# Performance work log

Hardware: AMD Instinct MI355X
Metric: run time of the kernel (lower is better)

Reference implementation:

```python
import jax, jax.numpy as jnp
import numpy as np

C = 1.0          # curvature
EPS = 1e-6
BETA = 0.5       # residual_beta
N_NODES = 65536
N_EDGES = 1048576
D = 128          # pure feature dim; hyperboloid coords are D+1


def _mink_dot(x, y):
    # Lorentz inner product <x,y>_L = -x0*y0 + sum_i xi*yi
    return jnp.sum(x * y, axis=-1) - 2.0 * x[..., 0] * y[..., 0]


def _proj(x, c=C):
    # project onto hyperboloid: x0 = sqrt(1/c + ||x_s||^2)
    xs = x[..., 1:]
    x0 = jnp.sqrt(1.0 / c + jnp.sum(xs * xs, axis=-1, keepdims=True))
    return jnp.concatenate([x0, xs], axis=-1)


def _log0_pure(x, c=C):
    # log map at origin, returning the pure (spatial) tangent part (..., D)
    sc = jnp.sqrt(c)
    x0 = x[..., :1]
    xs = x[..., 1:]
    xn = jnp.sqrt(jnp.maximum(jnp.sum(xs * xs, axis=-1, keepdims=True), EPS * EPS))
    theta = jnp.arccosh(jnp.maximum(sc * x0, 1.0 + EPS))
    return (theta / (sc * xn)) * xs


def _exp0_pure(v, c=C):
    # exp map at origin from pure tangent vector v (..., D) -> (..., D+1)
    sc = jnp.sqrt(c)
    vn = jnp.sqrt(jnp.maximum(jnp.sum(v * v, axis=-1, keepdims=True), EPS * EPS))
    a = sc * vn
    x0 = jnp.cosh(a) / sc
    xs = jnp.sinh(a) * v / a
    return jnp.concatenate([x0, xs], axis=-1)


def _log(x, y, c=C):
    # general Lorentz log map log_x(y)
    sc = jnp.sqrt(c)
    alpha = jnp.maximum(-c * _mink_dot(x, y), 1.0 + EPS)[..., None]
    u = y - alpha * x
    un = jnp.sqrt(jnp.maximum(_mink_dot(u, u)[..., None], EPS * EPS))
    dist = jnp.arccosh(alpha) / sc
    return dist * u / un


def _exp(x, v, c=C):
    # general Lorentz exp map exp_x(v)
    sc = jnp.sqrt(c)
    vn = jnp.sqrt(jnp.maximum(_mink_dot(v, v)[..., None], EPS * EPS))
    a = sc * vn
    return jnp.cosh(a) * x + jnp.sinh(a) * v / a


def _hgcn_layer(x, src, dst, W, b):
    n = x.shape[0]
    # HyperbolicLinear (basepoint=origin): tangent linear map then exp back
    h = _exp0_pure(_log0_pure(x) @ W.T + b)
    # mean aggregation in tangent space at origin (self-loops already in src/dst)
    t = _log0_pure(h)                                   # (N, D)
    s = jax.ops.segment_sum(t[src], dst, num_segments=n)  # (N, D)
    cnt = jax.ops.segment_sum(jnp.ones((src.shape[0],), t.dtype), dst, num_segments=n)
    mean = s / jnp.maximum(cnt, 1.0)[:, None]
    agg = _proj(_exp0_pure(mean))                        # normalize_after_aggregation
    # hyperbolic ReLU (basepoint=origin)
    act = _exp0_pure(jax.nn.relu(_log0_pure(agg)))
    # geodesic residual: exp_residual(beta * log_residual(act))
    act = _exp(x, BETA * _log(x, act))
    return _proj(act)


def setup_inputs() -> dict:
    key = jax.random.key(0)
    k1, k2, k3, k4, k5, k6 = jax.random.split(key, 6)
    xs = 0.1 * jax.random.normal(k1, (N_NODES, D), dtype=jnp.float32)
    x = _proj(jnp.concatenate([jnp.zeros((N_NODES, 1), jnp.float32), xs], axis=-1))
    edge_index = jax.random.randint(k2, (2, N_EDGES), 0, N_NODES, dtype=jnp.int32)
    scale = 1.0 / np.sqrt(D)
    W1 = scale * jax.random.normal(k3, (D, D), dtype=jnp.float32)
    b1 = 0.01 * jax.random.normal(k4, (D,), dtype=jnp.float32)
    W2 = scale * jax.random.normal(k5, (D, D), dtype=jnp.float32)
    b2 = 0.01 * jax.random.normal(k6, (D,), dtype=jnp.float32)
    return {"x": x, "edge_index": edge_index, "W1": W1, "b1": b1, "W2": W2, "b2": b2}


def reference(x, edge_index, W1, b1, W2, b2):
    n = x.shape[0]
    loops = jnp.arange(n, dtype=edge_index.dtype)
    src = jnp.concatenate([edge_index[0], loops])
    dst = jnp.concatenate([edge_index[1], loops])
    h = _hgcn_layer(x, src, dst, W1, b1)
    h = _proj(h)  # normalize_between_layers
    h = _hgcn_layer(h, src, dst, W2, b2)
    return h
```

## Files before the change

kernel.cpp:

```cpp
#include <hip/hip_runtime.h>
#include <hip/hip_bf16.h>
#include <hip/hip_fp16.h>
#include <math.h>

#define NN 65536
#define NE 1048576
#define D 128
#define DP 129
#define EPSF 1e-6f
#define TILE 4096

typedef _Float16 half8 __attribute__((ext_vector_type(8)));
typedef float floatx16 __attribute__((ext_vector_type(16)));
typedef float floatx2 __attribute__((ext_vector_type(2)));

__device__ __forceinline__ float frcp(float x) { return __builtin_amdgcn_rcpf(x); }
__device__ __forceinline__ float fsqrt(float x) { return __builtin_amdgcn_sqrtf(x); }
__device__ __forceinline__ float facosh(float x) {
    return __logf(x + fsqrt(fmaxf(x * x - 1.0f, 0.0f)));
}


__global__ __launch_bounds__(256) void k_bzero(int* __restrict__ bcnt) {
    bcnt[threadIdx.x] = 0;
}

__global__ __launch_bounds__(256) void k_bhist(const int* __restrict__ dst, int E,
                                               int* __restrict__ bcnt) {
    __shared__ int lh[256];
    int t = threadIdx.x;
    lh[t] = 0;
    __syncthreads();
    int base = blockIdx.x * TILE;
    #pragma unroll
    for (int k = 0; k < 16; ++k) {
        int i = base + k * 256 + t;
        if (i < E) atomicAdd(&lh[dst[i] >> 8], 1);
    }
    __syncthreads();
    if (lh[t]) atomicAdd(&bcnt[t], lh[t]);
}

__global__ __launch_bounds__(256) void k_bscan(const int* __restrict__ bcnt,
                                               int* __restrict__ bbase,
                                               int* __restrict__ bcur) {
    __shared__ int sh[256];
    int t = threadIdx.x;
    int v = bcnt[t];
    sh[t] = v;
    __syncthreads();
    for (int o = 1; o < 256; o <<= 1) {
        int u = (t >= o) ? sh[t - o] : 0;
        __syncthreads();
        sh[t] += u;
        __syncthreads();
    }
    int ex = sh[t] - v;
    bbase[t] = ex;
    bcur[t] = ex;
}

__global__ __launch_bounds__(256) void k_bsplit(const int* __restrict__ src,
                                                const int* __restrict__ dst, int E,
                                                int* __restrict__ bcur,
                                                unsigned int* __restrict__ ebuf) {
    __shared__ int lh[256];
    __shared__ int gres[256];
    int t = threadIdx.x;
    lh[t] = 0;
    __syncthreads();
    int base = blockIdx.x * TILE;
    unsigned int pk[16];
    int bk[16], rk[16];
    #pragma unroll
    for (int k = 0; k < 16; ++k) {
        int i = base + k * 256 + t;
        if (i < E) {
            int d = dst[i];
            int b = d >> 8;
            bk[k] = b;
            pk[k] = ((unsigned)(d & 255) << 16) | (unsigned)src[i];
            rk[k] = atomicAdd(&lh[b], 1);
        } else {
            bk[k] = -1; rk[k] = 0; pk[k] = 0;
        }
    }
    __syncthreads();
    gres[t] = lh[t] ? atomicAdd(&bcur[t], lh[t]) : 0;
    __syncthreads();
    #pragma unroll
    for (int k = 0; k < 16; ++k) {
        if (bk[k] >= 0) ebuf[gres[bk[k]] + rk[k]] = pk[k];
    }
}

__global__ __launch_bounds__(256) void k_csr(const unsigned int* __restrict__ ebuf,
                                             const int* __restrict__ bcnt,
                                             const int* __restrict__ bbase,
                                             int* __restrict__ deg,
                                             int* __restrict__ off,
                                             int* __restrict__ ssrc) {
    __shared__ int lh[256];
    __shared__ int sc[256];
    __shared__ int lcur[256];
    int t = threadIdx.x;
    int b = blockIdx.x;
    int start = bbase[b];
    int cnt = bcnt[b];
    lh[t] = 0;
    __syncthreads();
    for (int i = t; i < cnt; i += 256) {
        unsigned int e = ebuf[start + i];
        atomicAdd(&lh[e >> 16], 1);
    }
    __syncthreads();
    int v = lh[t];
    sc[t] = v;
    __syncthreads();
    for (int o = 1; o < 256; o <<= 1) {
        int u = (t >= o) ? sc[t - o] : 0;
        __syncthreads();
        sc[t] += u;
        __syncthreads();
    }
    int ex = sc[t] - v;
    int node = (b << 8) + t;
    deg[node] = v;
    off[node] = start + ex;
    lcur[t] = ex;
    __syncthreads();
    for (int i = t; i < cnt; i += 256) {
        unsigned int e = ebuf[start + i];
        int d = e >> 16;
        int r = atomicAdd(&lcur[d], 1);
        ssrc[start + r] = (int)(e & 0xFFFFu);
    }
}

template <bool FROM_F16>
__global__ __launch_bounds__(256) void k_gemm(const float* __restrict__ x,
                                              const _Float16* __restrict__ y,
                                              const float* __restrict__ W,
                                              const float* __restrict__ bias,
                                              unsigned int* __restrict__ zw) {
    __shared__ _Float16 Ah[128 * 128];
    __shared__ _Float16 Wh[128 * 128];
    int t = threadIdx.x;
    int w = t >> 6;
    int l = t & 63;
    int j = l & 31;
    int hi = l >> 5;
    int r0 = blockIdx.x * 128;

    #pragma unroll
    for (int i = 0; i < 8; ++i) {
        int c = i * 256 + t;
        int row = c >> 4, slot = c & 15;
        const float4* wp = (const float4*)(W + row * 128 + slot * 8);
        float4 w0 = wp[0], w1 = wp[1];
        half8 hv;
        hv[0] = (_Float16)w0.x; hv[1] = (_Float16)w0.y;
        hv[2] = (_Float16)w0.z; hv[3] = (_Float16)w0.w;
        hv[4] = (_Float16)w1.x; hv[5] = (_Float16)w1.y;
        hv[6] = (_Float16)w1.z; hv[7] = (_Float16)w1.w;
        *(half8*)&Wh[row * 128 + ((slot ^ (row & 15)) << 3)] = hv;
    }

    if constexpr (FROM_F16) {
        #pragma unroll
        for (int i = 0; i < 8; ++i) {
            int c = i * 256 + t;
            int row = c >> 4, slot = c & 15;
            half8 hv = *(const half8*)(y + (size_t)(r0 + row) * 128 + slot * 8);
            *(half8*)&Ah[row * 128 + ((slot ^ (row & 15)) << 3)] = hv;
        }
    } else {
        for (int it = 0; it < 16; ++it) {
            int rl = w * 32 + it * 2 + hi;
            const float* xr = x + (size_t)(r0 + rl) * DP;
            float x0 = xr[0];
            float a0 = xr[1 + j];
            float a1 = xr[33 + j];
            float a2 = xr[65 + j];
            float a3 = xr[97 + j];
            float ss = a0 * a0 + a1 * a1 + a2 * a2 + a3 * a3;
            ss += __shfl_xor(ss, 1);
            ss += __shfl_xor(ss, 2);
            ss += __shfl_xor(ss, 4);
            ss += __shfl_xor(ss, 8);
            ss += __shfl_xor(ss, 16);
            float xn = fsqrt(fmaxf(ss, EPSF * EPSF));
            float theta = facosh(fmaxf(x0, 1.0f + EPSF));
            float f = theta * frcp(xn);
            int base = rl * 128;
            int swz = (rl & 15) << 3;
            Ah[base + ((j)      ^ swz)] = (_Float16)(f * a0);
            Ah[base + ((j + 32) ^ swz)] = (_Float16)(f * a1);
            Ah[base + ((j + 64) ^ swz)] = (_Float16)(f * a2);
            Ah[base + ((j + 96) ^ swz)] = (_Float16)(f * a3);
        }
    }
    __syncthreads();

    int rA = w * 32 + j;
    int swzj = (j & 15) << 3;
    const _Float16* Abase = &Ah[rA * 128];
    const _Float16* B0 = &Wh[(j)*128];
    const _Float16* B1 = &Wh[(j + 32) * 128];
    const _Float16* B2 = &Wh[(j + 64) * 128];
    const _Float16* B3 = &Wh[(j + 96) * 128];

    float bv0 = bias[j], bv1 = bias[j + 32], bv2 = bias[j + 64], bv3 = bias[j + 96];
    floatx16 acc0, acc1, acc2, acc3;
    #pragma unroll
    for (int q = 0; q < 16; ++q) {
        acc0[q] = bv0; acc1[q] = bv1; acc2[q] = bv2; acc3[q] = bv3;
    }

    #pragma unroll
    for (int ks = 0; ks < 8; ++ks) {
        int kh = (ks * 16 + hi * 8) ^ swzj;
        half8 a  = *(const half8*)(Abase + kh);
        half8 b0 = *(const half8*)(B0 + kh);
        half8 b1 = *(const half8*)(B1 + kh);
        half8 b2 = *(const half8*)(B2 + kh);
        half8 b3 = *(const half8*)(B3 + kh);
        acc0 = __builtin_amdgcn_mfma_f32_32x32x16_f16(a, b0, acc0, 0, 0, 0);
        acc1 = __builtin_amdgcn_mfma_f32_32x32x16_f16(a, b1, acc1, 0, 0, 0);
        acc2 = __builtin_amdgcn_mfma_f32_32x32x16_f16(a, b2, acc2, 0, 0, 0);
        acc3 = __builtin_amdgcn_mfma_f32_32x32x16_f16(a, b3, acc3, 0, 0, 0);
    }

    #pragma unroll
    for (int q = 0; q < 16; ++q) {
        int row = r0 + w * 32 + (q & 3) + 8 * (q >> 2) + 4 * hi;
        unsigned int u = 0;
        u = (unsigned int)__builtin_amdgcn_cvt_pk_fp8_f32(acc0[q], acc1[q], (int)u, false);
        u = (unsigned int)__builtin_amdgcn_cvt_pk_fp8_f32(acc2[q], acc3[q], (int)u, true);
        zw[(size_t)row * 32 + j] = u;
    }
}

template <bool WRITE_Y>
__global__ __launch_bounds__(256) void k_agg(const unsigned short* __restrict__ zs,
                                             const float* xin,
                                             const int* __restrict__ off,
                                             const int* __restrict__ deg,
                                             const int* __restrict__ ssrc,
                                             float* out,
                                             _Float16* __restrict__ y2) {
    int wave = threadIdx.x >> 6, lane = threadIdx.x & 63;
    int node = __builtin_amdgcn_readfirstlane(blockIdx.x * 4 + wave);
    int c0 = (lane >> 1) + ((lane & 1) << 6);

    floatx2 acc0 = __builtin_amdgcn_cvt_pk_f32_fp8((int)zs[(size_t)node * 64 + lane], false);
    floatx2 acc1 = {0.f, 0.f}, acc2 = {0.f, 0.f}, acc3 = {0.f, 0.f};

    int start = __builtin_amdgcn_readfirstlane(off[node]);
    int dg = __builtin_amdgcn_readfirstlane(deg[node]);

    for (int c = 0; c < dg; c += 64) {
        int rem = dg - c;
        int m = rem < 64 ? rem : 64;
        int sv = ssrc[start + c + lane];
        int j = 0;
        for (; j + 7 < m; j += 8) {
            int s0 = __builtin_amdgcn_readlane(sv, j + 0);
            int s1 = __builtin_amdgcn_readlane(sv, j + 1);
            int s2 = __builtin_amdgcn_readlane(sv, j + 2);
            int s3 = __builtin_amdgcn_readlane(sv, j + 3);
            int s4 = __builtin_amdgcn_readlane(sv, j + 4);
            int s5 = __builtin_amdgcn_readlane(sv, j + 5);
            int s6 = __builtin_amdgcn_readlane(sv, j + 6);
            int s7 = __builtin_amdgcn_readlane(sv, j + 7);
            floatx2 v0 = __builtin_amdgcn_cvt_pk_f32_fp8((int)zs[(size_t)s0 * 64 + lane], false);
            floatx2 v1 = __builtin_amdgcn_cvt_pk_f32_fp8((int)zs[(size_t)s1 * 64 + lane], false);
            floatx2 v2 = __builtin_amdgcn_cvt_pk_f32_fp8((int)zs[(size_t)s2 * 64 + lane], false);
            floatx2 v3 = __builtin_amdgcn_cvt_pk_f32_fp8((int)zs[(size_t)s3 * 64 + lane], false);
            floatx2 v4 = __builtin_amdgcn_cvt_pk_f32_fp8((int)zs[(size_t)s4 * 64 + lane], false);
            floatx2 v5 = __builtin_amdgcn_cvt_pk_f32_fp8((int)zs[(size_t)s5 * 64 + lane], false);
            floatx2 v6 = __builtin_amdgcn_cvt_pk_f32_fp8((int)zs[(size_t)s6 * 64 + lane], false);
            floatx2 v7 = __builtin_amdgcn_cvt_pk_f32_fp8((int)zs[(size_t)s7 * 64 + lane], false);
            acc0 += v0; acc1 += v1; acc2 += v2; acc3 += v3;
            acc0 += v4; acc1 += v5; acc2 += v6; acc3 += v7;
        }
        for (; j < m; ++j) {
            int s = __builtin_amdgcn_readlane(sv, j);
            floatx2 v = __builtin_amdgcn_cvt_pk_f32_fp8((int)zs[(size_t)s * 64 + lane], false);
            acc0 += v;
        }
    }
    floatx2 accT = (acc0 + acc1) + (acc2 + acc3);
    float ax = accT.x, ay = accT.y;

    float inv = frcp((float)(dg + 1));
    float rx = fmaxf(ax * inv, 0.0f);
    float ry = fmaxf(ay * inv, 0.0f);

    float ss = rx * rx + ry * ry;
    #pragma unroll
    for (int o = 1; o < 64; o <<= 1) ss += __shfl_xor(ss, o);
    float av = fsqrt(fmaxf(ss, EPSF * EPSF));
    float t1 = __expf(av);
    float t1i = frcp(t1);
    float shf = 0.5f * (t1 - t1i) * frcp(av);
    float act0 = 0.5f * (t1 + t1i);
    float asx = shf * rx, asy = shf * ry;

    const float* xr = xin + (size_t)node * DP;
    float x0 = xr[0];
    float xsx = xr[1 + c0];
    float xsy = xr[33 + c0];

    float dot = asx * xsx + asy * xsy;
    #pragma unroll
    for (int o = 1; o < 64; o <<= 1) dot += __shfl_xor(dot, o);
    float mink = dot - act0 * x0;
    float alpha = fmaxf(-mink, 1.0f + EPSF);

    float u0 = act0 - alpha * x0;
    float ux = asx - alpha * xsx;
    float uy = asy - alpha * xsy;
    float uss = ux * ux + uy * uy;
    #pragma unroll
    for (int o = 1; o < 64; o <<= 1) uss += __shfl_xor(uss, o);
    float uu = uss - u0 * u0;
    float un = fsqrt(fmaxf(uu, EPSF * EPSF));

    float d = facosh(alpha);
    float a2 = 0.5f * d;
    float t2 = __expf(a2);
    float t2i = frcp(t2);
    float ch2 = 0.5f * (t2 + t2i);
    float sh2 = 0.5f * (t2 - t2i) * frcp(un);

    float ox = ch2 * xsx + sh2 * ux;
    float oy = ch2 * xsy + sh2 * uy;

    float os = ox * ox + oy * oy;
    #pragma unroll
    for (int o = 1; o < 64; o <<= 1) os += __shfl_xor(os, o);
    float p0 = fsqrt(1.0f + os);

    float* orow = out + (size_t)node * DP;
    if (lane == 0) orow[0] = p0;
    orow[1 + c0] = ox;
    orow[33 + c0] = oy;

    if constexpr (WRITE_Y) {
        float theta2 = facosh(fmaxf(p0, 1.0f + EPSF));
        float invn = frcp(fsqrt(fmaxf(os, EPSF * EPSF)));
        float f2 = theta2 * invn;
        _Float16* yr = y2 + (size_t)node * 128;
        yr[c0] = (_Float16)(f2 * ox);
        yr[c0 + 32] = (_Float16)(f2 * oy);
    }
}

extern "C" void kernel_launch(void* const* d_in, const int* in_sizes, int n_in,
                              void* d_out, int out_size, void* d_ws, size_t ws_size,
                              hipStream_t stream) {
    const float* x  = (const float*)d_in[0];
    const int* ei   = (const int*)d_in[1];
    const float* W1 = (const float*)d_in[2];
    const float* b1 = (const float*)d_in[3];
    const float* W2 = (const float*)d_in[4];
    const float* b2 = (const float*)d_in[5];
    float* out = (float*)d_out;

    int n = in_sizes[0] / DP;
    int E = in_sizes[1] / 2;
    const int* src = ei;
    const int* dst = ei + E;

    char* w = (char*)d_ws;
    unsigned char* z8 = (unsigned char*)w; w += (size_t)n * D;
    _Float16* y2 = (_Float16*)w;   w += (size_t)n * D * sizeof(_Float16);
    int* deg    = (int*)w;         w += (size_t)n * sizeof(int);
    int* off    = (int*)w;         w += (size_t)n * sizeof(int);
    int* ssrc   = (int*)w;         w += ((size_t)E + 64) * sizeof(int);
    unsigned int* ebuf = (unsigned int*)w; w += (size_t)E * sizeof(unsigned int);
    int* bcnt   = (int*)w;         w += 256 * sizeof(int);
    int* bbase  = (int*)w;         w += 256 * sizeof(int);
    int* bcur   = (int*)w;         w += 256 * sizeof(int);

    int tb = (E + TILE - 1) / TILE;

    k_bzero<<<1, 256, 0, stream>>>(bcnt);
    k_bhist<<<tb, 256, 0, stream>>>(dst, E, bcnt);
    k_bscan<<<1, 256, 0, stream>>>(bcnt, bbase, bcur);
    k_bsplit<<<tb, 256, 0, stream>>>(src, dst, E, bcur, ebuf);
    k_csr<<<256, 256, 0, stream>>>(ebuf, bcnt, bbase, deg, off, ssrc);

    k_gemm<false><<<n / 128, 256, 0, stream>>>(x, nullptr, W1, b1, (unsigned int*)z8);
    k_agg<true><<<n / 4, 256, 0, stream>>>((const unsigned short*)z8, x, off, deg, ssrc, out, y2);

    k_gemm<true><<<n / 128, 256, 0, stream>>>(nullptr, y2, W2, b2, (unsigned int*)z8);
    k_agg<false><<<n / 4, 256, 0, stream>>>((const unsigned short*)z8, out, off, deg, ssrc, out, nullptr);
}
```

Measured before the change: 243.9 us.

## Gather two neighbor rows per wave with dword loads in aggregation

The aggregation kernel now reads each 128-byte fp8 neighbor row as 32 dwords, with the two half-waves fetching different neighbors at once. Before, each lane loaded a 16-bit value from a single neighbor. This halves the number of gather load instructions per edge and doubles the work per load. The cost is a cross-half shuffle to combine partial sums, a 32-lane reduction layout, and half the wave sitting idle during the epilogue writes.

```diff
diff --git a/kernel.cpp b/kernel.cpp
--- a/kernel.cpp
+++ b/kernel.cpp
@@ -242,7 +242,7 @@
 }
 
 template <bool WRITE_Y>
-__global__ __launch_bounds__(256) void k_agg(const unsigned short* __restrict__ zs,
+__global__ __launch_bounds__(256) void k_agg(const unsigned int* __restrict__ zw,
                                              const float* xin,
                                              const int* __restrict__ off,
                                              const int* __restrict__ deg,
@@ -251,10 +251,13 @@
                                              _Float16* __restrict__ y2) {
     int wave = threadIdx.x >> 6, lane = threadIdx.x & 63;
     int node = __builtin_amdgcn_readfirstlane(blockIdx.x * 4 + wave);
-    int c0 = (lane >> 1) + ((lane & 1) << 6);
-
-    floatx2 acc0 = __builtin_amdgcn_cvt_pk_f32_fp8((int)zs[(size_t)node * 64 + lane], false);
-    floatx2 acc1 = {0.f, 0.f}, acc2 = {0.f, 0.f}, acc3 = {0.f, 0.f};
+    int wl = lane & 31;
+    bool hiH = lane >= 32;
+
+    unsigned int dwS = zw[(size_t)node * 32 + wl];
+
+    floatx2 a0 = {0.f, 0.f}, a1 = {0.f, 0.f};
+    floatx2 b0 = {0.f, 0.f}, b1 = {0.f, 0.f};
 
     int start = __builtin_amdgcn_readfirstlane(off[node]);
     int dg = __builtin_amdgcn_readfirstlane(deg[node]);
@@ -273,57 +276,87 @@
             int s5 = __builtin_amdgcn_readlane(sv, j + 5);
             int s6 = __builtin_amdgcn_readlane(sv, j + 6);
             int s7 = __builtin_amdgcn_readlane(sv, j + 7);
-            floatx2 v0 = __builtin_amdgcn_cvt_pk_f32_fp8((int)zs[(size_t)s0 * 64 + lane], false);
-            floatx2 v1 = __builtin_amdgcn_cvt_pk_f32_fp8((int)zs[(size_t)s1 * 64 + lane], false);
-            floatx2 v2 = __builtin_amdgcn_cvt_pk_f32_fp8((int)zs[(size_t)s2 * 64 + lane], false);
-            floatx2 v3 = __builtin_amdgcn_cvt_pk_f32_fp8((int)zs[(size_t)s3 * 64 + lane], false);
-            floatx2 v4 = __builtin_amdgcn_cvt_pk_f32_fp8((int)zs[(size_t)s4 * 64 + lane], false);
-            floatx2 v5 = __builtin_amdgcn_cvt_pk_f32_fp8((int)zs[(size_t)s5 * 64 + lane], false);
-            floatx2 v6 = __builtin_amdgcn_cvt_pk_f32_fp8((int)zs[(size_t)s6 * 64 + lane], false);
-            floatx2 v7 = __builtin_amdgcn_cvt_pk_f32_fp8((int)zs[(size_t)s7 * 64 + lane], false);
-            acc0 += v0; acc1 += v1; acc2 += v2; acc3 += v3;
-            acc0 += v4; acc1 += v5; acc2 += v6; acc3 += v7;
-        }
-        for (; j < m; ++j) {
+            int r0 = hiH ? s1 : s0;
+            int r1 = hiH ? s3 : s2;
+            int r2 = hiH ? s5 : s4;
+            int r3 = hiH ? s7 : s6;
+            unsigned int d0 = zw[(size_t)r0 * 32 + wl];
+            unsigned int d1 = zw[(size_t)r1 * 32 + wl];
+            unsigned int d2 = zw[(size_t)r2 * 32 + wl];
+            unsigned int d3 = zw[(size_t)r3 * 32 + wl];
+            a0 += __builtin_amdgcn_cvt_pk_f32_fp8((int)d0, false);
+            b0 += __builtin_amdgcn_cvt_pk_f32_fp8((int)d0, true);
+            a1 += __builtin_amdgcn_cvt_pk_f32_fp8((int)d1, false);
+            b1 += __builtin_amdgcn_cvt_pk_f32_fp8((int)d1, true);
+            a0 += __builtin_amdgcn_cvt_pk_f32_fp8((int)d2, false);
+            b0 += __builtin_amdgcn_cvt_pk_f32_fp8((int)d2, true);
+            a1 += __builtin_amdgcn_cvt_pk_f32_fp8((int)d3, false);
+            b1 += __builtin_amdgcn_cvt_pk_f32_fp8((int)d3, true);
+        }
+        for (; j + 1 < m; j += 2) {
+            int sA = __builtin_amdgcn_readlane(sv, j);
+            int sB = __builtin_amdgcn_readlane(sv, j + 1);
+            int r = hiH ? sB : sA;
+            unsigned int dw = zw[(size_t)r * 32 + wl];
+            a0 += __builtin_amdgcn_cvt_pk_f32_fp8((int)dw, false);
+            b0 += __builtin_amdgcn_cvt_pk_f32_fp8((int)dw, true);
+        }
+        if (j < m) {
             int s = __builtin_amdgcn_readlane(sv, j);
-            floatx2 v = __builtin_amdgcn_cvt_pk_f32_fp8((int)zs[(size_t)s * 64 + lane], false);
-            acc0 += v;
-        }
-    }
-    floatx2 accT = (acc0 + acc1) + (acc2 + acc3);
-    float ax = accT.x, ay = accT.y;
+            unsigned int dw = zw[(size_t)s * 32 + wl];
+            floatx2 va = __builtin_amdgcn_cvt_pk_f32_fp8((int)dw, false);
+            floatx2 vb = __builtin_amdgcn_cvt_pk_f32_fp8((int)dw, true);
+            if (hiH) { va.x = 0.f; va.y = 0.f; vb.x = 0.f; vb.y = 0.f; }
+            a1 += va;
+            b1 += vb;
+        }
+    }
+    floatx2 accA = a0 + a1;
+    floatx2 accB = b0 + b1;
+    accA.x += __shfl_xor(accA.x, 32);
+    accA.y += __shfl_xor(accA.y, 32);
+    accB.x += __shfl_xor(accB.x, 32);
+    accB.y += __shfl_xor(accB.y, 32);
+    accA += __builtin_amdgcn_cvt_pk_f32_fp8((int)dwS, false);
+    accB += __builtin_amdgcn_cvt_pk_f32_fp8((int)dwS, true);
 
     float inv = frcp((float)(dg + 1));
-    float rx = fmaxf(ax * inv, 0.0f);
-    float ry = fmaxf(ay * inv, 0.0f);
-
-    float ss = rx * rx + ry * ry;
-    #pragma unroll
-    for (int o = 1; o < 64; o <<= 1) ss += __shfl_xor(ss, o);
+    float r0m = fmaxf(accA.x * inv, 0.0f);
+    float r1m = fmaxf(accA.y * inv, 0.0f);
+    float r2m = fmaxf(accB.x * inv, 0.0f);
+    float r3m = fmaxf(accB.y * inv, 0.0f);
+
+    float ss = r0m * r0m + r1m * r1m + r2m * r2m + r3m * r3m;
+    #pragma unroll
+    for (int o = 1; o < 32; o <<= 1) ss += __shfl_xor(ss, o);
     float av = fsqrt(fmaxf(ss, EPSF * EPSF));
     float t1 = __expf(av);
     float t1i = frcp(t1);
     float shf = 0.5f * (t1 - t1i) * frcp(av);
     float act0 = 0.5f * (t1 + t1i);
-    float asx = shf * rx, asy = shf * ry;
+    float as0 = shf * r0m, as1 = shf * r1m, as2 = shf * r2m, as3 = shf * r3m;
 
     const float* xr = xin + (size_t)node * DP;
     float x0 = xr[0];
-    float xsx = xr[1 + c0];
-    float xsy = xr[33 + c0];
-
-    float dot = asx * xsx + asy * xsy;
-    #pragma unroll
-    for (int o = 1; o < 64; o <<= 1) dot += __shfl_xor(dot, o);
+    float xs0 = xr[1 + wl];
+    float xs1 = xr[33 + wl];
+    float xs2 = xr[65 + wl];
+    float xs3 = xr[97 + wl];
+
+    float dot = as0 * xs0 + as1 * xs1 + as2 * xs2 + as3 * xs3;
+    #pragma unroll
+    for (int o = 1; o < 32; o <<= 1) dot += __shfl_xor(dot, o);
     float mink = dot - act0 * x0;
     float alpha = fmaxf(-mink, 1.0f + EPSF);
 
     float u0 = act0 - alpha * x0;
-    float ux = asx - alpha * xsx;
-    float uy = asy - alpha * xsy;
-    float uss = ux * ux + uy * uy;
-    #pragma unroll
-    for (int o = 1; o < 64; o <<= 1) uss += __shfl_xor(uss, o);
+    float uv0 = as0 - alpha * xs0;
+    float uv1 = as1 - alpha * xs1;
+    float uv2 = as2 - alpha * xs2;
+    float uv3 = as3 - alpha * xs3;
+    float uss = uv0 * uv0 + uv1 * uv1 + uv2 * uv2 + uv3 * uv3;
+    #pragma unroll
+    for (int o = 1; o < 32; o <<= 1) uss += __shfl_xor(uss, o);
     float uu = uss - u0 * u0;
     float un = fsqrt(fmaxf(uu, EPSF * EPSF));
 
@@ -334,26 +367,34 @@
     float ch2 = 0.5f * (t2 + t2i);
     float sh2 = 0.5f * (t2 - t2i) * frcp(un);
 
-    float ox = ch2 * xsx + sh2 * ux;
-    float oy = ch2 * xsy + sh2 * uy;
-
-    float os = ox * ox + oy * oy;
-    #pragma unroll
-    for (int o = 1; o < 64; o <<= 1) os += __shfl_xor(os, o);
+    float o0 = ch2 * xs0 + sh2 * uv0;
+    float o1 = ch2 * xs1 + sh2 * uv1;
+    float o2 = ch2 * xs2 + sh2 * uv2;
+    float o3 = ch2 * xs3 + sh2 * uv3;
+
+    float os = o0 * o0 + o1 * o1 + o2 * o2 + o3 * o3;
+    #pragma unroll
+    for (int o = 1; o < 32; o <<= 1) os += __shfl_xor(os, o);
     float p0 = fsqrt(1.0f + os);
 
-    float* orow = out + (size_t)node * DP;
-    if (lane == 0) orow[0] = p0;
-    orow[1 + c0] = ox;
-    orow[33 + c0] = oy;
-
-    if constexpr (WRITE_Y) {
-        float theta2 = facosh(fmaxf(p0, 1.0f + EPSF));
-        float invn = frcp(fsqrt(fmaxf(os, EPSF * EPSF)));
-        float f2 = theta2 * invn;
-        _Float16* yr = y2 + (size_t)node * 128;
-        yr[c0] = (_Float16)(f2 * ox);
-        yr[c0 + 32] = (_Float16)(f2 * oy);
+    if (!hiH) {
+        float* orow = out + (size_t)node * DP;
+        if (wl == 0) orow[0] = p0;
+        orow[1 + wl] = o0;
+        orow[33 + wl] = o1;
+        orow[65 + wl] = o2;
+        orow[97 + wl] = o3;
+
+        if constexpr (WRITE_Y) {
+            float theta2 = facosh(fmaxf(p0, 1.0f + EPSF));
+            float invn = frcp(fsqrt(fmaxf(os, EPSF * EPSF)));
+            float f2 = theta2 * invn;
+            _Float16* yr = y2 + (size_t)node * 128;
+            yr[wl] = (_Float16)(f2 * o0);
+            yr[wl + 32] = (_Float16)(f2 * o1);
+            yr[wl + 64] = (_Float16)(f2 * o2);
+            yr[wl + 96] = (_Float16)(f2 * o3);
+        }
     }
 }
 
@@ -393,8 +434,8 @@
     k_csr<<<256, 256, 0, stream>>>(ebuf, bcnt, bbase, deg, off, ssrc);
 
     k_gemm<false><<<n / 128, 256, 0, stream>>>(x, nullptr, W1, b1, (unsigned int*)z8);
-    k_agg<true><<<n / 4, 256, 0, stream>>>((const unsigned short*)z8, x, off, deg, ssrc, out, y2);
+    k_agg<true><<<n / 4, 256, 0, stream>>>((const unsigned int*)z8, x, off, deg, ssrc, out, y2);
 
     k_gemm<true><<<n / 128, 256, 0, stream>>>(nullptr, y2, W2, b2, (unsigned int*)z8);
-    k_agg<false><<<n / 4, 256, 0, stream>>>((const unsigned short*)z8, out, off, deg, ssrc, out, nullptr);
-}
+    k_agg<false><<<n / 4, 256, 0, stream>>>((const unsigned int*)z8, out, off, deg, ssrc, out, nullptr);
+}
```

Result: faster. 237.0 us (-2.8%).
